# Kernel tuning notes

Measured on AMD Instinct MI355X. Metric: run time of the kernel, lower is better.

## Reference

```python
import jax, jax.numpy as jnp
import numpy as np

NUM_CLASSES = 80
TOPK = 9
EPS_OVERLAPS = 1e-6  # mmdet BboxOverlaps2D: union clamped to eps
EPS_YOLOV6 = 1e-9    # yolov6_iou_calculator: eps added to union


def _pairwise_iou(b1, b2, eps, add_eps):
    # b1: (..., M, 4), b2: (..., N, 4) xyxy -> (..., M, N)
    lt = jnp.maximum(b1[..., :, None, :2], b2[..., None, :, :2])
    rb = jnp.minimum(b1[..., :, None, 2:], b2[..., None, :, 2:])
    wh = jnp.clip(rb - lt, 0.0)
    overlap = wh[..., 0] * wh[..., 1]
    a1 = (b1[..., 2] - b1[..., 0]) * (b1[..., 3] - b1[..., 1])
    a2 = (b2[..., 2] - b2[..., 0]) * (b2[..., 3] - b2[..., 1])
    union = a1[..., :, None] + a2[..., None, :] - overlap
    return overlap / (union + eps) if add_eps else overlap / jnp.maximum(union, eps)


def _assign(pred_bboxes, priors, gt_labels, gt_bboxes, pad_bbox_flag, num_level_priors):
    num_level_priors = tuple(int(n) for n in np.asarray(num_level_priors))
    # priors (x, y, stride_w, stride_h) -> 5*stride cell boxes in xyxy
    cell_half = priors[:, 2:] * 2.5
    prior_boxes = jnp.concatenate([priors[:, :2] - cell_half, priors[:, :2] + cell_half], axis=-1)
    bs, num_gt = gt_bboxes.shape[0], gt_bboxes.shape[1]
    num_priors = priors.shape[0]
    gt_flat = gt_bboxes.reshape(-1, 4)

    # step 1: IoU between all priors and all gts
    overlaps = _pairwise_iou(gt_flat, prior_boxes, EPS_OVERLAPS, False).reshape(bs, num_gt, num_priors)

    # step 2: center distances
    gt_cxy = (gt_flat[:, :2] + gt_flat[:, 2:]) * 0.5
    prior_cxy = (prior_boxes[:, :2] + prior_boxes[:, 2:]) * 0.5
    dist = jnp.sqrt(jnp.sum((gt_cxy[:, None, :] - prior_cxy[None, :, :]) ** 2, axis=-1))
    dist = dist.reshape(bs, num_gt, num_priors)

    # step 3: per-level topk closest candidates
    pad_bool = pad_bbox_flag[..., 0] > 0  # (bs, num_gt)
    b_ix = jnp.arange(bs)[:, None, None]
    g_ix = jnp.arange(num_gt)[None, :, None]
    is_in_list, cand_list = [], []
    start = 0
    for pl in num_level_priors:
        k = min(TOPK, pl)
        d_l = jax.lax.dynamic_slice_in_dim(dist, start, pl, axis=-1)
        _, idx = jax.lax.top_k(-d_l, k)  # (bs, num_gt, k) smallest distances
        cand_list.append(idx + start)
        idx_m = jnp.where(pad_bool[..., None], idx, 0)
        counts = jnp.zeros((bs, num_gt, pl), dist.dtype).at[b_ix, g_ix, idx_m].add(1.0)
        is_in_list.append(jnp.where(counts > 1, jnp.zeros_like(counts), counts))
        start += pl
    is_in_candidate = jnp.concatenate(is_in_list, axis=-1)   # (bs, num_gt, num_priors)
    candidate_idxs = jnp.concatenate(cand_list, axis=-1)     # (bs, num_gt, k*levels)

    # step 4: mean + std of candidate IoUs as threshold
    candidate_overlaps = jnp.where(is_in_candidate > 0, overlaps, jnp.zeros_like(overlaps))
    gathered = jnp.take_along_axis(candidate_overlaps, candidate_idxs, axis=-1)
    thr = jnp.mean(gathered, axis=-1, keepdims=True) + jnp.std(gathered, axis=-1, keepdims=True, ddof=1)

    # step 5: keep candidates above threshold
    is_pos = jnp.where(candidate_overlaps > thr, is_in_candidate, jnp.zeros_like(is_in_candidate))

    # step 6: center of prior must lie inside gt box
    lt = prior_cxy[None, None, :, :] - gt_bboxes[:, :, None, :2]
    rb = gt_bboxes[:, :, None, 2:] - prior_cxy[None, None, :, :]
    is_in_gts = (jnp.minimum(lt, rb).min(axis=-1) > 1e-9).astype(gt_bboxes.dtype)

    pos_mask = is_pos * is_in_gts * pad_bbox_flag  # pad flag broadcasts (bs,num_gt,1)

    # resolve priors assigned to multiple gts: keep highest IoU gt
    fg = pos_mask.sum(axis=-2)  # (bs, num_priors)
    best_gt = jnp.argmax(overlaps, axis=1)  # (bs, num_priors)
    is_max = jax.nn.one_hot(best_gt, num_gt, dtype=pos_mask.dtype).transpose(0, 2, 1)
    pos_mask = jnp.where(fg[:, None, :] > 1, is_max, pos_mask)
    fg_mask = pos_mask.sum(axis=-2)                 # (bs, num_priors)
    gt_idx = jnp.argmax(pos_mask, axis=-2)          # (bs, num_priors)

    # targets
    flat_idx = gt_idx + jnp.arange(bs)[:, None] * num_gt
    assigned_labels = gt_labels.reshape(-1)[flat_idx]
    assigned_labels = jnp.where(fg_mask > 0, assigned_labels, NUM_CLASSES)
    assigned_bboxes = gt_bboxes.reshape(-1, 4)[flat_idx]
    assigned_scores = jax.nn.one_hot(assigned_labels, NUM_CLASSES + 1, dtype=gt_bboxes.dtype)[..., :NUM_CLASSES]

    # weight scores by IoU with predictions
    ious = _pairwise_iou(gt_bboxes, pred_bboxes, EPS_YOLOV6, True) * pos_mask
    assigned_scores = assigned_scores * jnp.max(ious, axis=-2)[..., None]
    return assigned_labels, assigned_bboxes, assigned_scores, fg_mask > 0


def setup_inputs() -> dict:
    key = jax.random.key(0)
    k0, k1, k2, k3, k4 = jax.random.split(key, 5)
    bs, num_gt, img = 32, 64, 640
    strides = (8, 16, 32)
    pri = []
    for s in strides:
        n = img // s
        xs = (np.arange(n, dtype=np.float32) + 0.5) * s
        gy, gx = np.meshgrid(xs, xs, indexing='ij')
        pts = np.stack([gx.ravel(), gy.ravel()], axis=1)
        st = np.full((pts.shape[0], 2), s, dtype=np.float32)
        pri.append(np.concatenate([pts, st], axis=1))
    priors = jnp.asarray(np.concatenate(pri, axis=0))  # (8400, 4)
    num_level_priors = (6400, 1600, 400)
    num_priors = priors.shape[0]
    cxy = jax.random.uniform(k0, (bs, num_gt, 2), minval=50.0, maxval=590.0)
    wh = jax.random.uniform(k1, (bs, num_gt, 2), minval=20.0, maxval=200.0)
    gt_bboxes = jnp.concatenate([cxy - wh * 0.5, cxy + wh * 0.5], axis=-1)
    gt_labels = jax.random.randint(k2, (bs, num_gt, 1), 0, NUM_CLASSES)
    pad_bbox_flag = jnp.ones((bs, num_gt, 1), jnp.float32)
    pcxy = priors[None, :, :2] + jax.random.normal(k3, (bs, num_priors, 2)) * 4.0
    pwh = jax.random.uniform(k4, (bs, num_priors, 2), minval=10.0, maxval=150.0)
    pred_bboxes = jnp.concatenate([pcxy - pwh * 0.5, pcxy + pwh * 0.5], axis=-1)
    return {'pred_bboxes': pred_bboxes, 'priors': priors, 'gt_labels': gt_labels,
            'gt_bboxes': gt_bboxes, 'pad_bbox_flag': pad_bbox_flag,
            'num_level_priors': num_level_priors}


def reference(pred_bboxes, priors, gt_labels, gt_bboxes, pad_bbox_flag, num_level_priors):
    return _assign(pred_bboxes, priors, gt_labels, gt_bboxes, pad_bbox_flag, num_level_priors)
```

## Files before the change

### kernel.cpp

```cpp
#include <hip/hip_runtime.h>

#define BS 32
#define NG 64
#define NP 8400
#define NTOPK 9
#define NUM_CLASSES 80
#define NCAND 27

__global__ __launch_bounds__(64) void k_candidates(
    const float4* __restrict__ gt_bboxes,
    const float*  __restrict__ pad_flag,
    unsigned long long* __restrict__ posbits
) {
    const int bg = blockIdx.x * 64 + threadIdx.x;
    const int b  = bg >> 6;
    const int g  = bg & 63;

    const float4 gt  = gt_bboxes[bg];
    const float  pad = pad_flag[bg];
    const float  gcx = (gt.x + gt.z) * 0.5f;
    const float  gcy = (gt.y + gt.w) * 0.5f;
    const float  garea = (gt.z - gt.x) * (gt.w - gt.y);

    const float lvl_s[3] = {8.0f, 16.0f, 32.0f};
    const int   lvl_n[3] = {80, 40, 20};
    const int   lvl_b[3] = {0, 6400, 8000};

    float ov[NCAND];
    int   ixs[NCAND];

    float sum = 0.0f;

    #pragma unroll
    for (int L = 0; L < 3; ++L) {
        const float s    = lvl_s[L];
        const int   n    = lvl_n[L];
        const int   base = lvl_b[L];

        int wx = (int)floorf(gcx / s) - 2;
        int wy = (int)floorf(gcy / s) - 2;
        wx = min(max(wx, 0), n - 5);
        wy = min(max(wy, 0), n - 5);

        unsigned long long loc[NTOPK];
        #pragma unroll
        for (int q = 0; q < NTOPK; ++q) loc[q] = ~0ull;

        #pragma unroll
        for (int dy = 0; dy < 5; ++dy) {
            const int   iy  = wy + dy;
            const float py  = ((float)iy + 0.5f) * s;
            const float ddy = gcy - py;
            #pragma unroll
            for (int dx = 0; dx < 5; ++dx) {
                const int   ix  = wx + dx;
                const float px  = ((float)ix + 0.5f) * s;
                const float ddx = gcx - px;
                const float d   = sqrtf(ddx * ddx + ddy * ddy);
                unsigned long long k =
                    ((unsigned long long)__float_as_uint(d) << 32) |
                    (unsigned int)(base + iy * n + ix);
                if (k < loc[NTOPK - 1]) {
                    loc[NTOPK - 1] = k;
                    #pragma unroll
                    for (int q = NTOPK - 1; q > 0; --q) {
                        unsigned long long lo = loc[q - 1], hi = loc[q];
                        bool sw = hi < lo;
                        loc[q - 1] = sw ? hi : lo;
                        loc[q]     = sw ? lo : hi;
                    }
                }
            }
        }

        const float hx = s * 2.5f;
        #pragma unroll
        for (int q = 0; q < NTOPK; ++q) {
            const int slot = L * NTOPK + q;
            const int idx  = (int)(loc[q] & 0xffffffffu);
            const int rel  = idx - base;
            const int iy   = rel / n;
            const int ix   = rel - iy * n;
            const float px = ((float)ix + 0.5f) * s;
            const float py = ((float)iy + 0.5f) * s;
            const float px0 = px - hx, py0 = py - hx;
            const float px1 = px + hx, py1 = py + hx;
            float lx = fmaxf(gt.x, px0), ly = fmaxf(gt.y, py0);
            float rx = fminf(gt.z, px1), ry = fminf(gt.w, py1);
            float w = fmaxf(rx - lx, 0.0f), h = fmaxf(ry - ly, 0.0f);
            float ovl = w * h;
            float parea = (px1 - px0) * (py1 - py0);
            float o = ovl / fmaxf(garea + parea - ovl, 1e-6f);
            ov[slot]  = o;
            ixs[slot] = idx;
            sum += o;
        }
    }

    const float mean = sum / (float)NCAND;
    float var = 0.0f;
    #pragma unroll
    for (int i = 0; i < NCAND; ++i) {
        float d = ov[i] - mean;
        var += d * d;
    }
    const float thr = mean + sqrtf(var / (float)(NCAND - 1));

    if (pad > 0.0f) {
        #pragma unroll
        for (int i = 0; i < NCAND; ++i) {
            if (ov[i] > thr) {
                const int   L    = i / NTOPK;
                const float s    = lvl_s[L];
                const int   n    = lvl_n[L];
                const int   base = lvl_b[L];
                const int idx = ixs[i];
                const int rel = idx - base;
                const int iy  = rel / n;
                const int ix  = rel - iy * n;
                const float px = ((float)ix + 0.5f) * s;
                const float py = ((float)iy + 0.5f) * s;
                float mm = fminf(fminf(px - gt.x, py - gt.y),
                                 fminf(gt.z - px, gt.w - py));
                if (mm > 1e-9f) {
                    atomicOr(&posbits[(size_t)b * NP + idx], 1ull << g);
                }
            }
        }
    }
}

__global__ __launch_bounds__(256) void k_assign(
    const float4* __restrict__ priors,
    const float4* __restrict__ gt_bboxes,
    const int*    __restrict__ gt_labels,
    const float4* __restrict__ pred_bboxes,
    const unsigned long long* __restrict__ posbits,
    float* __restrict__ out)
{
    __shared__ float4 s_gt[NG];
    __shared__ int    s_lab[NG];
    __shared__ int    s_plab[256];
    __shared__ float  s_piou[256];

    const int b   = blockIdx.y;
    const int tid = threadIdx.x;
    if (tid < NG) {
        s_gt[tid]  = gt_bboxes[b * NG + tid];
        s_lab[tid] = gt_labels[b * NG + tid];
    }
    __syncthreads();

    const int p0 = blockIdx.x * 256;
    const int p  = p0 + tid;
    int   label  = NUM_CLASSES;
    float iou_w  = 0.0f;

    if (p < NP) {
        const size_t bp = (size_t)b * NP + p;
        unsigned long long mask = posbits[bp];
        int fg = __popcll(mask);
        int gidx = 0;

        if (fg > 1) {
            float4 pr = priors[p];
            float hx = pr.z * 2.5f, hy = pr.w * 2.5f;
            float px0 = pr.x - hx, py0 = pr.y - hy, px1 = pr.x + hx, py1 = pr.y + hy;
            float parea = (px1 - px0) * (py1 - py0);
            float best = -1.0f;
            for (int gg = 0; gg < NG; ++gg) {
                float4 gtb = s_gt[gg];
                float lx = fmaxf(gtb.x, px0), ly = fmaxf(gtb.y, py0);
                float rx = fminf(gtb.z, px1), ry = fminf(gtb.w, py1);
                float w = fmaxf(rx - lx, 0.0f), h = fmaxf(ry - ly, 0.0f);
                float ovl = w * h;
                float ga = (gtb.z - gtb.x) * (gtb.w - gtb.y);
                float v = ovl / fmaxf(ga + parea - ovl, 1e-6f);
                if (v > best) { best = v; gidx = gg; }
            }
        } else if (fg == 1) {
            gidx = __ffsll((unsigned long long)mask) - 1;
        }

        const bool  fgm = fg > 0;
        const float4 gtb = s_gt[gidx];
        label = fgm ? s_lab[gidx] : NUM_CLASSES;

        if (fgm) {
            float4 pb = pred_bboxes[bp];
            float lx = fmaxf(gtb.x, pb.x), ly = fmaxf(gtb.y, pb.y);
            float rx = fminf(gtb.z, pb.z), ry = fminf(gtb.w, pb.w);
            float w = fmaxf(rx - lx, 0.0f), h = fmaxf(ry - ly, 0.0f);
            float ov = w * h;
            float ga = (gtb.z - gtb.x) * (gtb.w - gtb.y);
            float pa = (pb.z - pb.x) * (pb.w - pb.y);
            iou_w = ov / (ga + pa - ov + 1e-9f);
        }

        out[bp] = (float)label;
        ((float4*)(out + (size_t)BS * NP))[bp] = gtb;
        out[(size_t)BS * NP * 85 + bp] = fgm ? 1.0f : 0.0f;
    }

    s_plab[tid] = label;
    s_piou[tid] = iou_w;
    __syncthreads();

    const int npr  = min(256, NP - p0);
    const int nfl4 = npr * 20;
    float4* o4 = (float4*)(out + (size_t)BS * NP * 5 + ((size_t)b * NP + p0) * 80);
    for (int q = tid; q < nfl4; q += 256) {
        int pl   = q / 20;
        int comp = q - pl * 20;
        int lab  = s_plab[pl];
        float iw = s_piou[pl];
        int dd = lab - comp * 4;
        float4 v;
        v.x = (dd == 0) ? iw : 0.0f;
        v.y = (dd == 1) ? iw : 0.0f;
        v.z = (dd == 2) ? iw : 0.0f;
        v.w = (dd == 3) ? iw : 0.0f;
        o4[q] = v;
    }
}

extern "C" void kernel_launch(void* const* d_in, const int* in_sizes, int n_in,
                              void* d_out, int out_size, void* d_ws, size_t ws_size,
                              hipStream_t stream) {
    const float4* pred_bboxes = (const float4*)d_in[0];
    const float4* priors      = (const float4*)d_in[1];
    const int*    gt_labels   = (const int*)d_in[2];
    const float4* gt_bboxes   = (const float4*)d_in[3];
    const float*  pad_flag    = (const float*)d_in[4];

    unsigned long long* posbits = (unsigned long long*)d_ws;
    hipMemsetAsync(posbits, 0, (size_t)BS * NP * sizeof(unsigned long long), stream);

    k_candidates<<<dim3(BS * NG / 64), dim3(64), 0, stream>>>(
        gt_bboxes, pad_flag, posbits);

    k_assign<<<dim3((NP + 255) / 256, BS), dim3(256), 0, stream>>>(
        priors, gt_bboxes, gt_labels, pred_bboxes, posbits, (float*)d_out);
}
```

Measured before the change: 127.0 us.

## Fuse candidate selection into assignment kernel with shared-memory positive bitmasks

Removes the memset and the separate candidate kernel. Each assignment block now recomputes the per-gt top-k candidate selection and IoU thresholds in shared memory, with three levels spread across 192 threads, and sets positive bits only for priors in its own tile using shared atomics. This drops two launches, the global atomics and the posbits round trip through global memory. In exchange, every one of the 33×32 blocks redundantly recomputes the candidate work for all 64 gts, and the threshold step runs on only 64 threads.

Measured after the change: 128.0 us. No clear change (+0.8%).

```diff
diff --git a/kernel.cpp b/kernel.cpp
--- a/kernel.cpp
+++ b/kernel.cpp
@@ -7,158 +7,157 @@
 #define NUM_CLASSES 80
 #define NCAND 27
 
-__global__ __launch_bounds__(64) void k_candidates(
-    const float4* __restrict__ gt_bboxes,
-    const float*  __restrict__ pad_flag,
-    unsigned long long* __restrict__ posbits
-) {
-    const int bg = blockIdx.x * 64 + threadIdx.x;
-    const int b  = bg >> 6;
-    const int g  = bg & 63;
-
-    const float4 gt  = gt_bboxes[bg];
-    const float  pad = pad_flag[bg];
-    const float  gcx = (gt.x + gt.z) * 0.5f;
-    const float  gcy = (gt.y + gt.w) * 0.5f;
-    const float  garea = (gt.z - gt.x) * (gt.w - gt.y);
-
-    const float lvl_s[3] = {8.0f, 16.0f, 32.0f};
-    const int   lvl_n[3] = {80, 40, 20};
-    const int   lvl_b[3] = {0, 6400, 8000};
-
-    float ov[NCAND];
-    int   ixs[NCAND];
-
-    float sum = 0.0f;
-
-    #pragma unroll
-    for (int L = 0; L < 3; ++L) {
-        const float s    = lvl_s[L];
-        const int   n    = lvl_n[L];
-        const int   base = lvl_b[L];
-
-        int wx = (int)floorf(gcx / s) - 2;
-        int wy = (int)floorf(gcy / s) - 2;
-        wx = min(max(wx, 0), n - 5);
-        wy = min(max(wy, 0), n - 5);
-
-        unsigned long long loc[NTOPK];
-        #pragma unroll
-        for (int q = 0; q < NTOPK; ++q) loc[q] = ~0ull;
-
-        #pragma unroll
-        for (int dy = 0; dy < 5; ++dy) {
-            const int   iy  = wy + dy;
-            const float py  = ((float)iy + 0.5f) * s;
-            const float ddy = gcy - py;
-            #pragma unroll
-            for (int dx = 0; dx < 5; ++dx) {
-                const int   ix  = wx + dx;
-                const float px  = ((float)ix + 0.5f) * s;
-                const float ddx = gcx - px;
-                const float d   = sqrtf(ddx * ddx + ddy * ddy);
-                unsigned long long k =
-                    ((unsigned long long)__float_as_uint(d) << 32) |
-                    (unsigned int)(base + iy * n + ix);
-                if (k < loc[NTOPK - 1]) {
-                    loc[NTOPK - 1] = k;
-                    #pragma unroll
-                    for (int q = NTOPK - 1; q > 0; --q) {
-                        unsigned long long lo = loc[q - 1], hi = loc[q];
-                        bool sw = hi < lo;
-                        loc[q - 1] = sw ? hi : lo;
-                        loc[q]     = sw ? lo : hi;
-                    }
-                }
-            }
-        }
-
-        const float hx = s * 2.5f;
-        #pragma unroll
-        for (int q = 0; q < NTOPK; ++q) {
-            const int slot = L * NTOPK + q;
-            const int idx  = (int)(loc[q] & 0xffffffffu);
-            const int rel  = idx - base;
-            const int iy   = rel / n;
-            const int ix   = rel - iy * n;
-            const float px = ((float)ix + 0.5f) * s;
-            const float py = ((float)iy + 0.5f) * s;
-            const float px0 = px - hx, py0 = py - hx;
-            const float px1 = px + hx, py1 = py + hx;
-            float lx = fmaxf(gt.x, px0), ly = fmaxf(gt.y, py0);
-            float rx = fminf(gt.z, px1), ry = fminf(gt.w, py1);
-            float w = fmaxf(rx - lx, 0.0f), h = fmaxf(ry - ly, 0.0f);
-            float ovl = w * h;
-            float parea = (px1 - px0) * (py1 - py0);
-            float o = ovl / fmaxf(garea + parea - ovl, 1e-6f);
-            ov[slot]  = o;
-            ixs[slot] = idx;
-            sum += o;
-        }
-    }
-
-    const float mean = sum / (float)NCAND;
-    float var = 0.0f;
-    #pragma unroll
-    for (int i = 0; i < NCAND; ++i) {
-        float d = ov[i] - mean;
-        var += d * d;
-    }
-    const float thr = mean + sqrtf(var / (float)(NCAND - 1));
-
-    if (pad > 0.0f) {
-        #pragma unroll
-        for (int i = 0; i < NCAND; ++i) {
-            if (ov[i] > thr) {
-                const int   L    = i / NTOPK;
-                const float s    = lvl_s[L];
-                const int   n    = lvl_n[L];
-                const int   base = lvl_b[L];
-                const int idx = ixs[i];
-                const int rel = idx - base;
-                const int iy  = rel / n;
-                const int ix  = rel - iy * n;
-                const float px = ((float)ix + 0.5f) * s;
-                const float py = ((float)iy + 0.5f) * s;
-                float mm = fminf(fminf(px - gt.x, py - gt.y),
-                                 fminf(gt.z - px, gt.w - py));
-                if (mm > 1e-9f) {
-                    atomicOr(&posbits[(size_t)b * NP + idx], 1ull << g);
-                }
-            }
-        }
-    }
-}
-
-__global__ __launch_bounds__(256) void k_assign(
+__global__ __launch_bounds__(256) void k_fused(
     const float4* __restrict__ priors,
     const float4* __restrict__ gt_bboxes,
     const int*    __restrict__ gt_labels,
+    const float*  __restrict__ pad_flag,
     const float4* __restrict__ pred_bboxes,
-    const unsigned long long* __restrict__ posbits,
     float* __restrict__ out)
 {
     __shared__ float4 s_gt[NG];
     __shared__ int    s_lab[NG];
+    __shared__ unsigned long long s_bits[256];
+    __shared__ float  s_cov[NCAND][NG];
+    __shared__ int    s_cix[NCAND][NG];
     __shared__ int    s_plab[256];
     __shared__ float  s_piou[256];
 
     const int b   = blockIdx.y;
     const int tid = threadIdx.x;
+    const int p0  = blockIdx.x * 256;
+    const int npr = min(256, NP - p0);
+
     if (tid < NG) {
         s_gt[tid]  = gt_bboxes[b * NG + tid];
         s_lab[tid] = gt_labels[b * NG + tid];
     }
-    __syncthreads();
-
-    const int p0 = blockIdx.x * 256;
-    const int p  = p0 + tid;
-    int   label  = NUM_CLASSES;
-    float iou_w  = 0.0f;
+    s_bits[tid] = 0ull;
+    __syncthreads();
+
+    {
+        const int g = tid & 63;
+        const int L = tid >> 6;
+        if (L < 3) {
+            const float lvl_s[3] = {8.0f, 16.0f, 32.0f};
+            const int   lvl_n[3] = {80, 40, 20};
+            const int   lvl_b[3] = {0, 6400, 8000};
+            const float s    = lvl_s[L];
+            const int   n    = lvl_n[L];
+            const int   base = lvl_b[L];
+
+            const float4 gt = s_gt[g];
+            const float gcx = (gt.x + gt.z) * 0.5f;
+            const float gcy = (gt.y + gt.w) * 0.5f;
+            const float garea = (gt.z - gt.x) * (gt.w - gt.y);
+
+            int wx = (int)floorf(gcx / s) - 2;
+            int wy = (int)floorf(gcy / s) - 2;
+            wx = min(max(wx, 0), n - 5);
+            wy = min(max(wy, 0), n - 5);
+
+            unsigned long long loc[NTOPK];
+            #pragma unroll
+            for (int q = 0; q < NTOPK; ++q) loc[q] = ~0ull;
+
+            #pragma unroll
+            for (int dy = 0; dy < 5; ++dy) {
+                const float py  = ((float)(wy + dy) + 0.5f) * s;
+                const float ddy = gcy - py;
+                #pragma unroll
+                for (int dx = 0; dx < 5; ++dx) {
+                    const float px  = ((float)(wx + dx) + 0.5f) * s;
+                    const float ddx = gcx - px;
+                    const float d   = sqrtf(ddx * ddx + ddy * ddy);
+                    unsigned long long k =
+                        ((unsigned long long)__float_as_uint(d) << 32) |
+                        (unsigned int)(dy * 5 + dx);
+                    if (k < loc[NTOPK - 1]) {
+                        loc[NTOPK - 1] = k;
+                        #pragma unroll
+                        for (int q = NTOPK - 1; q > 0; --q) {
+                            unsigned long long lo = loc[q - 1], hi = loc[q];
+                            bool sw = hi < lo;
+                            loc[q - 1] = sw ? hi : lo;
+                            loc[q]     = sw ? lo : hi;
+                        }
+                    }
+                }
+            }
+
+            const float hx = s * 2.5f;
+            #pragma unroll
+            for (int q = 0; q < NTOPK; ++q) {
+                const int code = (int)(loc[q] & 31u);
+                const int dy = code / 5, dx = code - dy * 5;
+                const int iy = wy + dy,  ix = wx + dx;
+                const float px = ((float)ix + 0.5f) * s;
+                const float py = ((float)iy + 0.5f) * s;
+                const float px0 = px - hx, py0 = py - hx;
+                const float px1 = px + hx, py1 = py + hx;
+                float lx = fmaxf(gt.x, px0), ly = fmaxf(gt.y, py0);
+                float rx = fminf(gt.z, px1), ry = fminf(gt.w, py1);
+                float w = fmaxf(rx - lx, 0.0f), h = fmaxf(ry - ly, 0.0f);
+                float ovl = w * h;
+                float parea = (px1 - px0) * (py1 - py0);
+                float o = ovl / fmaxf(garea + parea - ovl, 1e-6f);
+                s_cov[L * NTOPK + q][g] = o;
+                s_cix[L * NTOPK + q][g] = base + iy * n + ix;
+            }
+        }
+    }
+    __syncthreads();
+
+    if (tid < NG) {
+        const int g = tid;
+        const float4 gt  = s_gt[g];
+        const float  pad = pad_flag[b * NG + g];
+
+        float sum = 0.0f;
+        #pragma unroll
+        for (int i = 0; i < NCAND; ++i) sum += s_cov[i][g];
+        const float mean = sum / (float)NCAND;
+        float var = 0.0f;
+        #pragma unroll
+        for (int i = 0; i < NCAND; ++i) {
+            float d = s_cov[i][g] - mean;
+            var += d * d;
+        }
+        const float thr = mean + sqrtf(var / (float)(NCAND - 1));
+
+        if (pad > 0.0f) {
+            #pragma unroll
+            for (int i = 0; i < NCAND; ++i) {
+                const int idx = s_cix[i][g];
+                const int rel_p = idx - p0;
+                if (rel_p >= 0 && rel_p < npr && s_cov[i][g] > thr) {
+                    const int   L    = i / NTOPK;
+                    const float s    = (L == 0) ? 8.0f : (L == 1) ? 16.0f : 32.0f;
+                    const int   n    = (L == 0) ? 80   : (L == 1) ? 40    : 20;
+                    const int   base = (L == 0) ? 0    : (L == 1) ? 6400  : 8000;
+                    const int rel = idx - base;
+                    const int iy  = rel / n;
+                    const int ix  = rel - iy * n;
+                    const float px = ((float)ix + 0.5f) * s;
+                    const float py = ((float)iy + 0.5f) * s;
+                    float mm = fminf(fminf(px - gt.x, py - gt.y),
+                                     fminf(gt.z - px, gt.w - py));
+                    if (mm > 1e-9f) {
+                        atomicOr(&s_bits[rel_p], 1ull << g);
+                    }
+                }
+            }
+        }
+    }
+    __syncthreads();
+
+    const int p = p0 + tid;
+    int   label = NUM_CLASSES;
+    float iou_w = 0.0f;
 
     if (p < NP) {
         const size_t bp = (size_t)b * NP + p;
-        unsigned long long mask = posbits[bp];
+        unsigned long long mask = s_bits[tid];
         int fg = __popcll(mask);
         int gidx = 0;
 
@@ -206,7 +205,6 @@
     s_piou[tid] = iou_w;
     __syncthreads();
 
-    const int npr  = min(256, NP - p0);
     const int nfl4 = npr * 20;
     float4* o4 = (float4*)(out + (size_t)BS * NP * 5 + ((size_t)b * NP + p0) * 80);
     for (int q = tid; q < nfl4; q += 256) {
@@ -233,12 +231,6 @@
     const float4* gt_bboxes   = (const float4*)d_in[3];
     const float*  pad_flag    = (const float*)d_in[4];
 
-    unsigned long long* posbits = (unsigned long long*)d_ws;
-    hipMemsetAsync(posbits, 0, (size_t)BS * NP * sizeof(unsigned long long), stream);
-
-    k_candidates<<<dim3(BS * NG / 64), dim3(64), 0, stream>>>(
-        gt_bboxes, pad_flag, posbits);
-
-    k_assign<<<dim3((NP + 255) / 256, BS), dim3(256), 0, stream>>>(
-        priors, gt_bboxes, gt_labels, pred_bboxes, posbits, (float*)d_out);
+    k_fused<<<dim3((NP + 255) / 256, BS), dim3(256), 0, stream>>>(
+        priors, gt_bboxes, gt_labels, pad_flag, pred_bboxes, (float*)d_out);
 }
```

## Split assignment kernel into resolve and write passes via intermediate records

Applied to the files above, without the earlier changes.

Splits the per-prior assignment kernel into two. The first resolves the gt index, label, IoU weight and foreground flag into a float4 record in workspace. The second reads the records and performs the large output writes, including the 80-class one-hot scores, with a launch-bounds occupancy hint. The aim is to keep the heavy store pass free of the register pressure and divergence of the 64-gt IoU argmax loop, at the cost of an extra launch and a workspace round-trip. It also replaces the level-table lookups in the candidate kernel with selects.

Measured after the change: 145.6 us. +14.6%, slower.

```diff
diff --git a/kernel.cpp b/kernel.cpp
--- a/kernel.cpp
+++ b/kernel.cpp
@@ -28,7 +28,6 @@
 
     float ov[NCAND];
     int   ixs[NCAND];
-
     float sum = 0.0f;
 
     #pragma unroll
@@ -100,10 +99,7 @@
     const float mean = sum / (float)NCAND;
     float var = 0.0f;
     #pragma unroll
-    for (int i = 0; i < NCAND; ++i) {
-        float d = ov[i] - mean;
-        var += d * d;
-    }
+    for (int i = 0; i < NCAND; ++i) { float d = ov[i] - mean; var += d * d; }
     const float thr = mean + sqrtf(var / (float)(NCAND - 1));
 
     if (pad > 0.0f) {
@@ -111,9 +107,9 @@
         for (int i = 0; i < NCAND; ++i) {
             if (ov[i] > thr) {
                 const int   L    = i / NTOPK;
-                const float s    = lvl_s[L];
-                const int   n    = lvl_n[L];
-                const int   base = lvl_b[L];
+                const float s    = (L == 0) ? 8.0f : (L == 1) ? 16.0f : 32.0f;
+                const int   n    = (L == 0) ? 80   : (L == 1) ? 40    : 20;
+                const int   base = (L == 0) ? 0    : (L == 1) ? 6400  : 8000;
                 const int idx = ixs[i];
                 const int rel = idx - base;
                 const int iy  = rel / n;
@@ -130,18 +126,16 @@
     }
 }
 
-__global__ __launch_bounds__(256) void k_assign(
+__global__ __launch_bounds__(256) void k_resolve(
     const float4* __restrict__ priors,
     const float4* __restrict__ gt_bboxes,
     const int*    __restrict__ gt_labels,
     const float4* __restrict__ pred_bboxes,
     const unsigned long long* __restrict__ posbits,
-    float* __restrict__ out)
+    float4* __restrict__ records)
 {
     __shared__ float4 s_gt[NG];
     __shared__ int    s_lab[NG];
-    __shared__ int    s_plab[256];
-    __shared__ float  s_piou[256];
 
     const int b   = blockIdx.y;
     const int tid = threadIdx.x;
@@ -151,62 +145,96 @@
     }
     __syncthreads();
 
-    const int p0 = blockIdx.x * 256;
-    const int p  = p0 + tid;
-    int   label  = NUM_CLASSES;
-    float iou_w  = 0.0f;
+    const int p = blockIdx.x * 256 + tid;
+    if (p >= NP) return;
+    const size_t bp = (size_t)b * NP + p;
+
+    unsigned long long mask = posbits[bp];
+    int fg = __popcll(mask);
+    int gidx = 0;
+
+    if (fg > 1) {
+        float4 pr = priors[p];
+        float hx = pr.z * 2.5f, hy = pr.w * 2.5f;
+        float px0 = pr.x - hx, py0 = pr.y - hy, px1 = pr.x + hx, py1 = pr.y + hy;
+        float parea = (px1 - px0) * (py1 - py0);
+        float best = -1.0f;
+        for (int gg = 0; gg < NG; ++gg) {
+            float4 gtb = s_gt[gg];
+            float lx = fmaxf(gtb.x, px0), ly = fmaxf(gtb.y, py0);
+            float rx = fminf(gtb.z, px1), ry = fminf(gtb.w, py1);
+            float w = fmaxf(rx - lx, 0.0f), h = fmaxf(ry - ly, 0.0f);
+            float ovl = w * h;
+            float ga = (gtb.z - gtb.x) * (gtb.w - gtb.y);
+            float v = ovl / fmaxf(ga + parea - ovl, 1e-6f);
+            if (v > best) { best = v; gidx = gg; }
+        }
+    } else if (fg == 1) {
+        gidx = __ffsll((unsigned long long)mask) - 1;
+    }
+
+    const bool fgm  = fg > 0;
+    const int label = fgm ? s_lab[gidx] : NUM_CLASSES;
+
+    float iou_w = 0.0f;
+    if (fgm) {
+        float4 gtb = s_gt[gidx];
+        float4 pb  = pred_bboxes[bp];
+        float lx = fmaxf(gtb.x, pb.x), ly = fmaxf(gtb.y, pb.y);
+        float rx = fminf(gtb.z, pb.z), ry = fminf(gtb.w, pb.w);
+        float w = fmaxf(rx - lx, 0.0f), h = fmaxf(ry - ly, 0.0f);
+        float ov = w * h;
+        float ga = (gtb.z - gtb.x) * (gtb.w - gtb.y);
+        float pa = (pb.z - pb.x) * (pb.w - pb.y);
+        iou_w = ov / (ga + pa - ov + 1e-9f);
+    }
+
+    float4 rec;
+    rec.x = __int_as_float(gidx);
+    rec.y = __int_as_float(label);
+    rec.z = iou_w;
+    rec.w = fgm ? 1.0f : 0.0f;
+    records[bp] = rec;
+}
+
+__global__ __launch_bounds__(256, 8) void k_write(
+    const float4* __restrict__ gt_bboxes,
+    const float4* __restrict__ records,
+    float* __restrict__ out)
+{
+    __shared__ float4 s_gt[NG];
+    __shared__ int    s_plab[256];
+    __shared__ float  s_piou[256];
+
+    const int b   = blockIdx.y;
+    const int tid = threadIdx.x;
+    const int p0  = blockIdx.x * 256;
+    const int npr = min(256, NP - p0);
+
+    if (tid < NG) s_gt[tid] = gt_bboxes[b * NG + tid];
+
+    int   label = NUM_CLASSES;
+    float iou_w = 0.0f;
+    const int p = p0 + tid;
 
     if (p < NP) {
         const size_t bp = (size_t)b * NP + p;
-        unsigned long long mask = posbits[bp];
-        int fg = __popcll(mask);
-        int gidx = 0;
-
-        if (fg > 1) {
-            float4 pr = priors[p];
-            float hx = pr.z * 2.5f, hy = pr.w * 2.5f;
-            float px0 = pr.x - hx, py0 = pr.y - hy, px1 = pr.x + hx, py1 = pr.y + hy;
-            float parea = (px1 - px0) * (py1 - py0);
-            float best = -1.0f;
-            for (int gg = 0; gg < NG; ++gg) {
-                float4 gtb = s_gt[gg];
-                float lx = fmaxf(gtb.x, px0), ly = fmaxf(gtb.y, py0);
-                float rx = fminf(gtb.z, px1), ry = fminf(gtb.w, py1);
-                float w = fmaxf(rx - lx, 0.0f), h = fmaxf(ry - ly, 0.0f);
-                float ovl = w * h;
-                float ga = (gtb.z - gtb.x) * (gtb.w - gtb.y);
-                float v = ovl / fmaxf(ga + parea - ovl, 1e-6f);
-                if (v > best) { best = v; gidx = gg; }
-            }
-        } else if (fg == 1) {
-            gidx = __ffsll((unsigned long long)mask) - 1;
-        }
-
-        const bool  fgm = fg > 0;
-        const float4 gtb = s_gt[gidx];
-        label = fgm ? s_lab[gidx] : NUM_CLASSES;
-
-        if (fgm) {
-            float4 pb = pred_bboxes[bp];
-            float lx = fmaxf(gtb.x, pb.x), ly = fmaxf(gtb.y, pb.y);
-            float rx = fminf(gtb.z, pb.z), ry = fminf(gtb.w, pb.w);
-            float w = fmaxf(rx - lx, 0.0f), h = fmaxf(ry - ly, 0.0f);
-            float ov = w * h;
-            float ga = (gtb.z - gtb.x) * (gtb.w - gtb.y);
-            float pa = (pb.z - pb.x) * (pb.w - pb.y);
-            iou_w = ov / (ga + pa - ov + 1e-9f);
-        }
-
+        float4 rec = records[bp];
+        const int gidx = __float_as_int(rec.x);
+        label = __float_as_int(rec.y);
+        iou_w = rec.z;
+        __syncthreads();
         out[bp] = (float)label;
-        ((float4*)(out + (size_t)BS * NP))[bp] = gtb;
-        out[(size_t)BS * NP * 85 + bp] = fgm ? 1.0f : 0.0f;
+        ((float4*)(out + (size_t)BS * NP))[bp] = s_gt[gidx];
+        out[(size_t)BS * NP * 85 + bp] = rec.w;
+    } else {
+        __syncthreads();
     }
 
     s_plab[tid] = label;
     s_piou[tid] = iou_w;
     __syncthreads();
 
-    const int npr  = min(256, NP - p0);
     const int nfl4 = npr * 20;
     float4* o4 = (float4*)(out + (size_t)BS * NP * 5 + ((size_t)b * NP + p0) * 80);
     for (int q = tid; q < nfl4; q += 256) {
@@ -234,11 +262,16 @@
     const float*  pad_flag    = (const float*)d_in[4];
 
     unsigned long long* posbits = (unsigned long long*)d_ws;
+    float4* records = (float4*)((char*)d_ws + (size_t)BS * NP * 8);
+
     hipMemsetAsync(posbits, 0, (size_t)BS * NP * sizeof(unsigned long long), stream);
 
     k_candidates<<<dim3(BS * NG / 64), dim3(64), 0, stream>>>(
         gt_bboxes, pad_flag, posbits);
 
-    k_assign<<<dim3((NP + 255) / 256, BS), dim3(256), 0, stream>>>(
-        priors, gt_bboxes, gt_labels, pred_bboxes, posbits, (float*)d_out);
-}
+    k_resolve<<<dim3((NP + 255) / 256, BS), dim3(256), 0, stream>>>(
+        priors, gt_bboxes, gt_labels, pred_bboxes, posbits, records);
+
+    k_write<<<dim3((NP + 255) / 256, BS), dim3(256), 0, stream>>>(
+        gt_bboxes, records, (float*)d_out);
+}
```

## Assign one wavefront per gt in candidate kernel, lanes issue atomics

Applied to the files above, without the earlier changes.

The candidate-selection kernel now runs one 64-lane wavefront per (batch, gt) pair instead of one thread per pair. Every lane redundantly computes the top-k and the IoU statistics, and each of the first 27 lanes keeps one candidate and issues its atomicOr in parallel. This replaces the serial per-thread atomic loop with divergent branches and spreads 2048 work items over 512 blocks instead of 32. The trade is 64x redundant arithmetic per gt, which is hidden by the wavefront running in lockstep.

New measurement: 135.2 us. 1.06x slower.

```diff
diff --git a/kernel.cpp b/kernel.cpp
--- a/kernel.cpp
+++ b/kernel.cpp
@@ -7,14 +7,16 @@
 #define NUM_CLASSES 80
 #define NCAND 27
 
-__global__ __launch_bounds__(64) void k_candidates(
+__global__ __launch_bounds__(256) void k_candidates(
     const float4* __restrict__ gt_bboxes,
     const float*  __restrict__ pad_flag,
     unsigned long long* __restrict__ posbits
 ) {
-    const int bg = blockIdx.x * 64 + threadIdx.x;
-    const int b  = bg >> 6;
-    const int g  = bg & 63;
+    const int tid  = threadIdx.x;
+    const int wave = tid >> 6, lane = tid & 63;
+    const int bg   = blockIdx.x * 4 + wave;
+    const int b    = bg >> 6;
+    const int g    = bg & 63;
 
     const float4 gt  = gt_bboxes[bg];
     const float  pad = pad_flag[bg];
@@ -27,9 +29,10 @@
     const int   lvl_b[3] = {0, 6400, 8000};
 
     float ov[NCAND];
-    int   ixs[NCAND];
-
     float sum = 0.0f;
+
+    float myov = 0.0f, mymm = -1.0f;
+    int   myix = 0;
 
     #pragma unroll
     for (int L = 0; L < 3; ++L) {
@@ -91,42 +94,22 @@
             float ovl = w * h;
             float parea = (px1 - px0) * (py1 - py0);
             float o = ovl / fmaxf(garea + parea - ovl, 1e-6f);
-            ov[slot]  = o;
-            ixs[slot] = idx;
+            ov[slot] = o;
             sum += o;
+            float mm = fminf(fminf(px - gt.x, py - gt.y),
+                             fminf(gt.z - px, gt.w - py));
+            if (lane == slot) { myov = o; myix = idx; mymm = mm; }
         }
     }
 
     const float mean = sum / (float)NCAND;
     float var = 0.0f;
     #pragma unroll
-    for (int i = 0; i < NCAND; ++i) {
-        float d = ov[i] - mean;
-        var += d * d;
-    }
+    for (int i = 0; i < NCAND; ++i) { float d = ov[i] - mean; var += d * d; }
     const float thr = mean + sqrtf(var / (float)(NCAND - 1));
 
-    if (pad > 0.0f) {
-        #pragma unroll
-        for (int i = 0; i < NCAND; ++i) {
-            if (ov[i] > thr) {
-                const int   L    = i / NTOPK;
-                const float s    = lvl_s[L];
-                const int   n    = lvl_n[L];
-                const int   base = lvl_b[L];
-                const int idx = ixs[i];
-                const int rel = idx - base;
-                const int iy  = rel / n;
-                const int ix  = rel - iy * n;
-                const float px = ((float)ix + 0.5f) * s;
-                const float py = ((float)iy + 0.5f) * s;
-                float mm = fminf(fminf(px - gt.x, py - gt.y),
-                                 fminf(gt.z - px, gt.w - py));
-                if (mm > 1e-9f) {
-                    atomicOr(&posbits[(size_t)b * NP + idx], 1ull << g);
-                }
-            }
-        }
+    if (lane < NCAND && pad > 0.0f && myov > thr && mymm > 1e-9f) {
+        atomicOr(&posbits[(size_t)b * NP + myix], 1ull << g);
     }
 }
 
@@ -236,7 +219,7 @@
     unsigned long long* posbits = (unsigned long long*)d_ws;
     hipMemsetAsync(posbits, 0, (size_t)BS * NP * sizeof(unsigned long long), stream);
 
-    k_candidates<<<dim3(BS * NG / 64), dim3(64), 0, stream>>>(
+    k_candidates<<<dim3(BS * NG / 4), dim3(256), 0, stream>>>(
         gt_bboxes, pad_flag, posbits);
 
     k_assign<<<dim3((NP + 255) / 256, BS), dim3(256), 0, stream>>>(
```
